# Performance work log

Hardware: AMD Instinct MI355X
Metric: run time of the kernel (lower is better)

The kernel has to match this reference:

```python
import jax, jax.numpy as jnp
import numpy as np

N = 50000   # query points
N2 = 50000  # key/value points
C = 128     # n_channels
G = 8       # n_groups
S = 16      # n_samples
CS = C // G # n_share_channels
EPS = 1e-5


def setup_inputs() -> dict:
    key = jax.random.key(0)
    ks = jax.random.split(key, 16)
    std = 0.02
    return {
        "p": jax.random.normal(ks[0], (N, 3), jnp.float32),
        "x": jax.random.normal(ks[1], (N, C), jnp.float32),
        "p2": jax.random.normal(ks[2], (N2, 3), jnp.float32),
        "x2": jax.random.normal(ks[3], (N2, C), jnp.float32),
        "idx": jax.random.randint(ks[4], (N, S), 0, N2, jnp.int32),
        "Wq": jax.random.normal(ks[5], (C, C), jnp.float32) * std,
        "bq": jnp.zeros((C,), jnp.float32),
        "Wk": jax.random.normal(ks[6], (C, C), jnp.float32) * std,
        "bk": jnp.zeros((C,), jnp.float32),
        "Wv": jax.random.normal(ks[7], (C, C), jnp.float32) * std,
        "bv": jnp.zeros((C,), jnp.float32),
        # linear_p: Conv1d(3,3,1) -> BN(3) -> ReLU -> Conv1d(3, 2G, 1)
        "W1": jax.random.normal(ks[8], (3, 3), jnp.float32) * 0.5,
        "b1": jnp.zeros((3,), jnp.float32),
        "bn_gamma": jnp.ones((3,), jnp.float32),
        "bn_beta": jnp.zeros((3,), jnp.float32),
        "bn_mean": jnp.zeros((3,), jnp.float32),
        "bn_var": jnp.ones((3,), jnp.float32),
        "W2": jax.random.normal(ks[9], (2 * G, 3), jnp.float32) * 0.5,
        "b2": jnp.zeros((2 * G,), jnp.float32),
    }


def reference(p, x, p2, x2, idx,
              Wq, bq, Wk, bk, Wv, bv,
              W1, b1, bn_gamma, bn_beta, bn_mean, bn_var, W2, b2):
    n = x.shape[0]
    # Q/K/V projections
    x_q = x @ Wq.T + bq                       # (n, C)
    x_k = (x2 @ Wk.T + bk)[idx]               # (n, S, C)  KNN gather
    x_v = (x2 @ Wv.T + bv)[idx]               # (n, S, C)
    # relative positions
    p_r = p2[idx] - p[:, None, :]             # (n, S, 3)
    # linear_p (pointwise convs == per-neighbor MLP over the 3 coord channels)
    h = p_r @ W1.T + b1
    h = (h - bn_mean) * jax.lax.rsqrt(bn_var + EPS) * bn_gamma + bn_beta
    h = jax.nn.relu(h)
    pe = h @ W2.T + b2                        # (n, S, 2G)
    p_rq, p_rk = jnp.split(pe, 2, axis=-1)    # each (n, S, G)
    # grouped attention
    k4 = x_k.reshape(n, S, G, CS) + p_rk[..., None]
    q4 = x_q.reshape(n, 1, G, CS) + p_rq[..., None]
    logits = jnp.sum(k4 * q4, axis=-1) / np.float32(np.sqrt(CS))  # (n, S, G)
    w = jax.nn.softmax(logits, axis=1)        # softmax over neighbors
    out = jnp.einsum('nsgc,nsg->ngc', x_v.reshape(n, S, G, CS), w)
    return out.reshape(n, C)
```

## Files before the change

### kernel.cpp

```cpp
#include <hip/hip_runtime.h>
#include <hip/hip_bf16.h>

#define NQ   50000
#define NKV  50000
#define CC   128
#define GG   8
#define SS   16
#define CSH  16

typedef short    bf16x8 __attribute__((ext_vector_type(8)));
typedef float    f32x4  __attribute__((ext_vector_type(4)));
typedef unsigned u32x4  __attribute__((ext_vector_type(4)));
typedef unsigned u32x2  __attribute__((ext_vector_type(2)));
typedef int      i32x4  __attribute__((ext_vector_type(4)));

__device__ __forceinline__ float bf_lo(unsigned u){ union{unsigned x; float f;} v; v.x = u << 16;        return v.f; }
__device__ __forceinline__ float bf_hi(unsigned u){ union{unsigned x; float f;} v; v.x = u & 0xffff0000u; return v.f; }
__device__ __forceinline__ unsigned short f2bfu(float f){
    __hip_bfloat16 h = __float2bfloat16(f);
    return *reinterpret_cast<unsigned short*>(&h);
}
__device__ __forceinline__ short f2bfs(float f){
    __hip_bfloat16 h = __float2bfloat16(f);
    return *reinterpret_cast<short*>(&h);
}

__device__ __forceinline__ void load16bf(const __hip_bfloat16* ptr, float* o){
    const u32x4* p4 = reinterpret_cast<const u32x4*>(ptr);
    u32x4 a = p4[0]; u32x4 b = p4[1];
    o[0]=bf_lo(a[0]);  o[1]=bf_hi(a[0]);  o[2]=bf_lo(a[1]);  o[3]=bf_hi(a[1]);
    o[4]=bf_lo(a[2]);  o[5]=bf_hi(a[2]);  o[6]=bf_lo(a[3]);  o[7]=bf_hi(a[3]);
    o[8]=bf_lo(b[0]);  o[9]=bf_hi(b[0]);  o[10]=bf_lo(b[1]); o[11]=bf_hi(b[1]);
    o[12]=bf_lo(b[2]); o[13]=bf_hi(b[2]); o[14]=bf_lo(b[3]); o[15]=bf_hi(b[3]);
}

__device__ __forceinline__ void load16bf_nt(const __hip_bfloat16* ptr, float* o){
    const u32x4* p4 = reinterpret_cast<const u32x4*>(ptr);
    u32x4 a = __builtin_nontemporal_load(p4);
    u32x4 b = __builtin_nontemporal_load(p4 + 1);
    o[0]=bf_lo(a[0]);  o[1]=bf_hi(a[0]);  o[2]=bf_lo(a[1]);  o[3]=bf_hi(a[1]);
    o[4]=bf_lo(a[2]);  o[5]=bf_hi(a[2]);  o[6]=bf_lo(a[3]);  o[7]=bf_hi(a[3]);
    o[8]=bf_lo(b[0]);  o[9]=bf_hi(b[0]);  o[10]=bf_lo(b[1]); o[11]=bf_hi(b[1]);
    o[12]=bf_lo(b[2]); o[13]=bf_hi(b[2]); o[14]=bf_lo(b[3]); o[15]=bf_hi(b[3]);
}

__device__ __forceinline__ bf16x8 cvt8(const float* p){
    const f32x4* q = reinterpret_cast<const f32x4*>(p);
    f32x4 u = q[0], v = q[1];
    bf16x8 r;
    r[0]=f2bfs(u[0]); r[1]=f2bfs(u[1]); r[2]=f2bfs(u[2]); r[3]=f2bfs(u[3]);
    r[4]=f2bfs(v[0]); r[5]=f2bfs(v[1]); r[6]=f2bfs(v[2]); r[7]=f2bfs(v[3]);
    return r;
}

__global__ __launch_bounds__(256) void qkv_gemm(
    const float* __restrict__ x,
    const float* __restrict__ x2,
    const float* __restrict__ Wq, const float* __restrict__ Wk,
    const float* __restrict__ Wv,
    const float* __restrict__ bq, const float* __restrict__ bk,
    const float* __restrict__ bv,
    __hip_bfloat16* __restrict__ Qf,
    __hip_bfloat16* __restrict__ KVf)
{
    __shared__ short lds16[16384];

    const int which = blockIdx.y;
    const float* src;  const float* W;  const float* bias;
    short* dstb; int dstride, hoff;
    if (which == 0)      { src = x;  W = Wq; bias = bq; dstb = (short*)Qf;  dstride = CC;     hoff = 0;  }
    else if (which == 1) { src = x2; W = Wk; bias = bk; dstb = (short*)KVf; dstride = 2 * CC; hoff = 0;  }
    else                 { src = x2; W = Wv; bias = bv; dstb = (short*)KVf; dstride = 2 * CC; hoff = CC; }
    const int nrows = NQ;

    const int tid = threadIdx.x;
    #pragma unroll
    for (int i = 0; i < 8; ++i) {
        const int o   = i * 2048 + tid * 8;
        const bf16x8 v = cvt8(W + o);
        const int row = o >> 7, col = o & 127;
        const int lchunk = (((row >> 4) * 4 + (col >> 5)) << 6)
                         + (((col >> 3) & 3) << 4) + (row & 15);
        *reinterpret_cast<bf16x8*>(&lds16[lchunk * 8]) = v;
    }

    const int wave = tid >> 6;
    const int lane = tid & 63;
    const int r  = lane & 15;
    const int kq = lane >> 4;
    const int base = blockIdx.x * 128 + wave * 32;

    bf16x8 bfrag[2][4];
    #pragma unroll
    for (int mt = 0; mt < 2; ++mt) {
        int row = base + mt * 16 + r;
        if (row >= nrows) row = nrows - 1;
        const float* xr = src + (size_t)row * CC + kq * 8;
        #pragma unroll
        for (int kb = 0; kb < 4; ++kb)
            bfrag[mt][kb] = cvt8(xr + kb * 32);
    }

    __syncthreads();

    #pragma unroll
    for (int t = 0; t < 8; ++t) {
        bf16x8 af[4];
        #pragma unroll
        for (int kb = 0; kb < 4; ++kb)
            af[kb] = *reinterpret_cast<const bf16x8*>(
                &lds16[(((t * 4 + kb) << 6) + lane) * 8]);

        f32x4 acc0 = {0.f,0.f,0.f,0.f}, acc1 = {0.f,0.f,0.f,0.f};
        #pragma unroll
        for (int kb = 0; kb < 4; ++kb) {
            acc0 = __builtin_amdgcn_mfma_f32_16x16x32_bf16(af[kb], bfrag[0][kb], acc0, 0, 0, 0);
            acc1 = __builtin_amdgcn_mfma_f32_16x16x32_bf16(af[kb], bfrag[1][kb], acc1, 0, 0, 0);
        }

        const f32x4 bi = *reinterpret_cast<const f32x4*>(bias + t * 16 + kq * 4);
        #pragma unroll
        for (int mt = 0; mt < 2; ++mt) {
            const int row = base + mt * 16 + r;
            if (row < nrows) {
                const f32x4 a = mt ? acc1 : acc0;
                u32x2 pk;
                pk[0] = (unsigned)f2bfu(a[0] + bi[0]) | ((unsigned)f2bfu(a[1] + bi[1]) << 16);
                pk[1] = (unsigned)f2bfu(a[2] + bi[2]) | ((unsigned)f2bfu(a[3] + bi[3]) << 16);
                __builtin_nontemporal_store(pk, reinterpret_cast<u32x2*>(
                    dstb + (size_t)row * dstride + hoff + t * 16 + kq * 4));
            }
        }
    }
}

__global__ __launch_bounds__(256) void attn_kernel(
    const float* __restrict__ p,
    const float* __restrict__ p2,
    const int*   __restrict__ idx,
    const float* __restrict__ W1,
    const float* __restrict__ b1,
    const float* __restrict__ bn_gamma,
    const float* __restrict__ bn_beta,
    const float* __restrict__ bn_mean,
    const float* __restrict__ bn_var,
    const float* __restrict__ W2,
    const float* __restrict__ b2,
    const __hip_bfloat16* __restrict__ Qf,
    const __hip_bfloat16* __restrict__ KVf,
    float* __restrict__ out)
{
    const int tid = blockIdx.x * 256 + threadIdx.x;
    if (tid >= NQ * GG) return;
    const int n = tid >> 3;
    const int g = tid & 7;

    float fw1[3][3], fb1[3];
    #pragma unroll
    for (int j = 0; j < 3; ++j) {
        const float sc = bn_gamma[j] * rsqrtf(bn_var[j] + 1e-5f);
        #pragma unroll
        for (int k = 0; k < 3; ++k) fw1[j][k] = W1[j*3 + k] * sc;
        fb1[j] = (b1[j] - bn_mean[j]) * sc + bn_beta[j];
    }
    const float w2q0 = W2[g*3+0],     w2q1 = W2[g*3+1],     w2q2 = W2[g*3+2];
    const float w2k0 = W2[(g+8)*3+0], w2k1 = W2[(g+8)*3+1], w2k2 = W2[(g+8)*3+2];
    const float b2q = b2[g], b2k = b2[g+8];

    const float px = p[(size_t)n*3+0];
    const float py = p[(size_t)n*3+1];
    const float pz = p[(size_t)n*3+2];

    int nbr[SS];
    {
        const i32x4* ip = reinterpret_cast<const i32x4*>(idx + (size_t)n * SS);
        i32x4 i0 = __builtin_nontemporal_load(ip);
        i32x4 i1 = __builtin_nontemporal_load(ip + 1);
        i32x4 i2 = __builtin_nontemporal_load(ip + 2);
        i32x4 i3 = __builtin_nontemporal_load(ip + 3);
        nbr[0]=i0[0]; nbr[1]=i0[1]; nbr[2]=i0[2]; nbr[3]=i0[3];
        nbr[4]=i1[0]; nbr[5]=i1[1]; nbr[6]=i1[2]; nbr[7]=i1[3];
        nbr[8]=i2[0]; nbr[9]=i2[1]; nbr[10]=i2[2]; nbr[11]=i2[3];
        nbr[12]=i3[0]; nbr[13]=i3[1]; nbr[14]=i3[2]; nbr[15]=i3[3];
    }

    float q[CSH];
    load16bf_nt(Qf + (size_t)n * CC + g * CSH, q);

    float acc[CSH];
    #pragma unroll
    for (int c = 0; c < CSH; ++c) acc[c] = 0.f;
    float sum = 0.f;
    float m = -3.0e38f;

    #pragma unroll 4
    for (int s = 0; s < SS; ++s) {
        const int i = nbr[s];
        const __hip_bfloat16* kv = KVf + (size_t)i * (2 * CC) + g * CSH;

        float kk[CSH], vv[CSH];
        load16bf(kv, kk);
        load16bf(kv + CC, vv);

        const float rx = p2[(size_t)i*3+0] - px;
        const float ry = p2[(size_t)i*3+1] - py;
        const float rz = p2[(size_t)i*3+2] - pz;
        const float h0 = fmaxf(fw1[0][0]*rx + fw1[0][1]*ry + fw1[0][2]*rz + fb1[0], 0.f);
        const float h1 = fmaxf(fw1[1][0]*rx + fw1[1][1]*ry + fw1[1][2]*rz + fb1[1], 0.f);
        const float h2 = fmaxf(fw1[2][0]*rx + fw1[2][1]*ry + fw1[2][2]*rz + fb1[2], 0.f);
        const float prq = w2q0*h0 + w2q1*h1 + w2q2*h2 + b2q;
        const float prk = w2k0*h0 + w2k1*h1 + w2k2*h2 + b2k;

        float d = 0.f;
        #pragma unroll
        for (int c = 0; c < CSH; ++c) d += (kk[c] + prk) * (q[c] + prq);
        d *= 0.25f;

        const float mnew = fmaxf(m, d);
        const float corr = __expf(m - mnew);
        const float w    = __expf(d - mnew);
        sum = sum * corr + w;
        #pragma unroll
        for (int c = 0; c < CSH; ++c) acc[c] = acc[c] * corr + w * vv[c];
        m = mnew;
    }

    const float inv = 1.f / sum;

    f32x4* op = reinterpret_cast<f32x4*>(out + (size_t)n * CC + g * CSH);
    f32x4 o0 = {acc[0]*inv,  acc[1]*inv,  acc[2]*inv,  acc[3]*inv};
    f32x4 o1 = {acc[4]*inv,  acc[5]*inv,  acc[6]*inv,  acc[7]*inv};
    f32x4 o2 = {acc[8]*inv,  acc[9]*inv,  acc[10]*inv, acc[11]*inv};
    f32x4 o3 = {acc[12]*inv, acc[13]*inv, acc[14]*inv, acc[15]*inv};
    __builtin_nontemporal_store(o0, op);
    __builtin_nontemporal_store(o1, op + 1);
    __builtin_nontemporal_store(o2, op + 2);
    __builtin_nontemporal_store(o3, op + 3);
}

extern "C" void kernel_launch(void* const* d_in, const int* in_sizes, int n_in,
                              void* d_out, int out_size, void* d_ws, size_t ws_size,
                              hipStream_t stream) {
    const float* p   = (const float*)d_in[0];
    const float* x   = (const float*)d_in[1];
    const float* p2  = (const float*)d_in[2];
    const float* x2  = (const float*)d_in[3];
    const int*   idx = (const int*)d_in[4];
    const float* Wq  = (const float*)d_in[5];
    const float* bq  = (const float*)d_in[6];
    const float* Wk  = (const float*)d_in[7];
    const float* bk  = (const float*)d_in[8];
    const float* Wv  = (const float*)d_in[9];
    const float* bv  = (const float*)d_in[10];
    const float* W1  = (const float*)d_in[11];
    const float* b1  = (const float*)d_in[12];
    const float* bng = (const float*)d_in[13];
    const float* bnb = (const float*)d_in[14];
    const float* bnm = (const float*)d_in[15];
    const float* bnv = (const float*)d_in[16];
    const float* W2  = (const float*)d_in[17];
    const float* b2  = (const float*)d_in[18];
    float* out = (float*)d_out;

    __hip_bfloat16* Qf  = (__hip_bfloat16*)d_ws;
    __hip_bfloat16* KVf = Qf + (size_t)NQ * CC;

    qkv_gemm<<<dim3(391, 3), 256, 0, stream>>>(
        x, x2, Wq, Wk, Wv, bq, bk, bv, Qf, KVf);

    const int nthreads = NQ * GG;
    attn_kernel<<<(nthreads + 255) / 256, 256, 0, stream>>>(
        p, p2, idx, W1, b1, bng, bnb, bnm, bnv, W2, b2, Qf, KVf, out);
}
```

Before: 230.1 us.

## Restructure QKV GEMM to share x2 fragments across K and V per block

The QKV projection kernel changes from a 3-way y-grid (one weight matrix per block) to a 1D grid where each block processes 64 rows and runs Q, K and V back to back. It restages each weight matrix in LDS between synchronisations, so x2 is read once for both K and V. Each wave now covers 16 rows instead of 32. Nontemporal loads and stores are also replaced with regular ones in both kernels, so the bf16 QKV intermediates stay cache-friendly for the gather. The cost is three serial weight stagings with barriers per block, which cuts per-block MFMA reuse of the A fragments.

```diff
diff --git a/kernel.cpp b/kernel.cpp
--- a/kernel.cpp
+++ b/kernel.cpp
@@ -28,16 +28,6 @@
 __device__ __forceinline__ void load16bf(const __hip_bfloat16* ptr, float* o){
     const u32x4* p4 = reinterpret_cast<const u32x4*>(ptr);
     u32x4 a = p4[0]; u32x4 b = p4[1];
-    o[0]=bf_lo(a[0]);  o[1]=bf_hi(a[0]);  o[2]=bf_lo(a[1]);  o[3]=bf_hi(a[1]);
-    o[4]=bf_lo(a[2]);  o[5]=bf_hi(a[2]);  o[6]=bf_lo(a[3]);  o[7]=bf_hi(a[3]);
-    o[8]=bf_lo(b[0]);  o[9]=bf_hi(b[0]);  o[10]=bf_lo(b[1]); o[11]=bf_hi(b[1]);
-    o[12]=bf_lo(b[2]); o[13]=bf_hi(b[2]); o[14]=bf_lo(b[3]); o[15]=bf_hi(b[3]);
-}
-
-__device__ __forceinline__ void load16bf_nt(const __hip_bfloat16* ptr, float* o){
-    const u32x4* p4 = reinterpret_cast<const u32x4*>(ptr);
-    u32x4 a = __builtin_nontemporal_load(p4);
-    u32x4 b = __builtin_nontemporal_load(p4 + 1);
     o[0]=bf_lo(a[0]);  o[1]=bf_hi(a[0]);  o[2]=bf_lo(a[1]);  o[3]=bf_hi(a[1]);
     o[4]=bf_lo(a[2]);  o[5]=bf_hi(a[2]);  o[6]=bf_lo(a[3]);  o[7]=bf_hi(a[3]);
     o[8]=bf_lo(b[0]);  o[9]=bf_hi(b[0]);  o[10]=bf_lo(b[1]); o[11]=bf_hi(b[1]);
@@ -65,73 +55,76 @@
 {
     __shared__ short lds16[16384];
 
-    const int which = blockIdx.y;
-    const float* src;  const float* W;  const float* bias;
-    short* dstb; int dstride, hoff;
-    if (which == 0)      { src = x;  W = Wq; bias = bq; dstb = (short*)Qf;  dstride = CC;     hoff = 0;  }
-    else if (which == 1) { src = x2; W = Wk; bias = bk; dstb = (short*)KVf; dstride = 2 * CC; hoff = 0;  }
-    else                 { src = x2; W = Wv; bias = bv; dstb = (short*)KVf; dstride = 2 * CC; hoff = CC; }
-    const int nrows = NQ;
-
-    const int tid = threadIdx.x;
-    #pragma unroll
-    for (int i = 0; i < 8; ++i) {
-        const int o   = i * 2048 + tid * 8;
-        const bf16x8 v = cvt8(W + o);
-        const int row = o >> 7, col = o & 127;
-        const int lchunk = (((row >> 4) * 4 + (col >> 5)) << 6)
-                         + (((col >> 3) & 3) << 4) + (row & 15);
-        *reinterpret_cast<bf16x8*>(&lds16[lchunk * 8]) = v;
-    }
-
+    const int tid  = threadIdx.x;
     const int wave = tid >> 6;
     const int lane = tid & 63;
-    const int r  = lane & 15;
-    const int kq = lane >> 4;
-    const int base = blockIdx.x * 128 + wave * 32;
-
-    bf16x8 bfrag[2][4];
-    #pragma unroll
-    for (int mt = 0; mt < 2; ++mt) {
-        int row = base + mt * 16 + r;
-        if (row >= nrows) row = nrows - 1;
+    const int r    = lane & 15;
+    const int kq   = lane >> 4;
+    const int wbase = blockIdx.x * 64 + wave * 16;
+
+    auto stageW = [&](const float* __restrict__ W){
+        #pragma unroll
+        for (int i = 0; i < 8; ++i) {
+            const int o   = i * 2048 + tid * 8;
+            const bf16x8 v = cvt8(W + o);
+            const int row = o >> 7, col = o & 127;
+            const int lchunk = (((row >> 4) * 4 + (col >> 5)) << 6)
+                             + (((col >> 3) & 3) << 4) + (row & 15);
+            *reinterpret_cast<bf16x8*>(&lds16[lchunk * 8]) = v;
+        }
+    };
+
+    auto loadB = [&](const float* __restrict__ src, bf16x8 (&bfrag)[4]){
+        int row = wbase + r;
+        if (row >= NQ) row = NQ - 1;
         const float* xr = src + (size_t)row * CC + kq * 8;
         #pragma unroll
         for (int kb = 0; kb < 4; ++kb)
-            bfrag[mt][kb] = cvt8(xr + kb * 32);
-    }
-
-    __syncthreads();
-
-    #pragma unroll
-    for (int t = 0; t < 8; ++t) {
-        bf16x8 af[4];
-        #pragma unroll
-        for (int kb = 0; kb < 4; ++kb)
-            af[kb] = *reinterpret_cast<const bf16x8*>(
-                &lds16[(((t * 4 + kb) << 6) + lane) * 8]);
-
-        f32x4 acc0 = {0.f,0.f,0.f,0.f}, acc1 = {0.f,0.f,0.f,0.f};
-        #pragma unroll
-        for (int kb = 0; kb < 4; ++kb) {
-            acc0 = __builtin_amdgcn_mfma_f32_16x16x32_bf16(af[kb], bfrag[0][kb], acc0, 0, 0, 0);
-            acc1 = __builtin_amdgcn_mfma_f32_16x16x32_bf16(af[kb], bfrag[1][kb], acc1, 0, 0, 0);
-        }
-
-        const f32x4 bi = *reinterpret_cast<const f32x4*>(bias + t * 16 + kq * 4);
-        #pragma unroll
-        for (int mt = 0; mt < 2; ++mt) {
-            const int row = base + mt * 16 + r;
-            if (row < nrows) {
-                const f32x4 a = mt ? acc1 : acc0;
+            bfrag[kb] = cvt8(xr + kb * 32);
+    };
+
+    auto runTiles = [&](const bf16x8 (&bfrag)[4], const float* __restrict__ bias,
+                        short* __restrict__ dstb, int dstride, int hoff){
+        const int row = wbase + r;
+        #pragma unroll
+        for (int t = 0; t < 8; ++t) {
+            bf16x8 af[4];
+            #pragma unroll
+            for (int kb = 0; kb < 4; ++kb)
+                af[kb] = *reinterpret_cast<const bf16x8*>(
+                    &lds16[(((t * 4 + kb) << 6) + lane) * 8]);
+
+            f32x4 acc = {0.f,0.f,0.f,0.f};
+            #pragma unroll
+            for (int kb = 0; kb < 4; ++kb)
+                acc = __builtin_amdgcn_mfma_f32_16x16x32_bf16(af[kb], bfrag[kb], acc, 0, 0, 0);
+
+            const f32x4 bi = *reinterpret_cast<const f32x4*>(bias + t * 16 + kq * 4);
+            if (row < NQ) {
                 u32x2 pk;
-                pk[0] = (unsigned)f2bfu(a[0] + bi[0]) | ((unsigned)f2bfu(a[1] + bi[1]) << 16);
-                pk[1] = (unsigned)f2bfu(a[2] + bi[2]) | ((unsigned)f2bfu(a[3] + bi[3]) << 16);
-                __builtin_nontemporal_store(pk, reinterpret_cast<u32x2*>(
-                    dstb + (size_t)row * dstride + hoff + t * 16 + kq * 4));
+                pk[0] = (unsigned)f2bfu(acc[0] + bi[0]) | ((unsigned)f2bfu(acc[1] + bi[1]) << 16);
+                pk[1] = (unsigned)f2bfu(acc[2] + bi[2]) | ((unsigned)f2bfu(acc[3] + bi[3]) << 16);
+                *reinterpret_cast<u32x2*>(
+                    dstb + (size_t)row * dstride + hoff + t * 16 + kq * 4) = pk;
             }
         }
-    }
+    };
+
+    bf16x8 fq[4], fkv[4];
+    loadB(x,  fq);
+    loadB(x2, fkv);
+
+    stageW(Wq);
+    __syncthreads();
+    runTiles(fq, bq, (short*)Qf, CC, 0);
+    __syncthreads();
+    stageW(Wk);
+    __syncthreads();
+    runTiles(fkv, bk, (short*)KVf, 2 * CC, 0);
+    __syncthreads();
+    stageW(Wv);
+    __syncthreads();
+    runTiles(fkv, bv, (short*)KVf, 2 * CC, CC);
 }
 
 __global__ __launch_bounds__(256) void attn_kernel(
@@ -174,10 +167,7 @@
     int nbr[SS];
     {
         const i32x4* ip = reinterpret_cast<const i32x4*>(idx + (size_t)n * SS);
-        i32x4 i0 = __builtin_nontemporal_load(ip);
-        i32x4 i1 = __builtin_nontemporal_load(ip + 1);
-        i32x4 i2 = __builtin_nontemporal_load(ip + 2);
-        i32x4 i3 = __builtin_nontemporal_load(ip + 3);
+        i32x4 i0 = ip[0], i1 = ip[1], i2 = ip[2], i3 = ip[3];
         nbr[0]=i0[0]; nbr[1]=i0[1]; nbr[2]=i0[2]; nbr[3]=i0[3];
         nbr[4]=i1[0]; nbr[5]=i1[1]; nbr[6]=i1[2]; nbr[7]=i1[3];
         nbr[8]=i2[0]; nbr[9]=i2[1]; nbr[10]=i2[2]; nbr[11]=i2[3];
@@ -185,7 +175,7 @@
     }
 
     float q[CSH];
-    load16bf_nt(Qf + (size_t)n * CC + g * CSH, q);
+    load16bf(Qf + (size_t)n * CC + g * CSH, q);
 
     float acc[CSH];
     #pragma unroll
@@ -232,10 +222,7 @@
     f32x4 o1 = {acc[4]*inv,  acc[5]*inv,  acc[6]*inv,  acc[7]*inv};
     f32x4 o2 = {acc[8]*inv,  acc[9]*inv,  acc[10]*inv, acc[11]*inv};
     f32x4 o3 = {acc[12]*inv, acc[13]*inv, acc[14]*inv, acc[15]*inv};
-    __builtin_nontemporal_store(o0, op);
-    __builtin_nontemporal_store(o1, op + 1);
-    __builtin_nontemporal_store(o2, op + 2);
-    __builtin_nontemporal_store(o3, op + 3);
+    op[0] = o0; op[1] = o1; op[2] = o2; op[3] = o3;
 }
 
 extern "C" void kernel_launch(void* const* d_in, const int* in_sizes, int n_in,
@@ -265,7 +252,7 @@
     __hip_bfloat16* Qf  = (__hip_bfloat16*)d_ws;
     __hip_bfloat16* KVf = Qf + (size_t)NQ * CC;
 
-    qkv_gemm<<<dim3(391, 3), 256, 0, stream>>>(
+    qkv_gemm<<<dim3(782), 256, 0, stream>>>(
         x, x2, Wq, Wk, Wv, bq, bk, bv, Qf, KVf);
 
     const int nthreads = NQ * GG;
```

After: 212.2 us. 1.08x faster.
